# Optimization experiments

Hardware: AMD Instinct MI355X
Metric: run time of the kernel (lower is better)

## Reference

```python
import jax, jax.numpy as jnp
import numpy as np

N_NODES = 100000
N_EDGES = 1600000
D = 64
N_TARGETS = 100
N_GRAPHS = 512


def gcn_conv(x, W, b, src, dst):
    """GCNConv with default add_self_loops=True, symmetric normalization."""
    n = x.shape[0]
    h = x @ W  # [N, out]
    ones = jnp.ones(dst.shape[0], dtype=h.dtype)
    deg = jax.ops.segment_sum(ones, dst, num_segments=n) + 1.0  # +1 for self-loop
    dinv = jax.lax.rsqrt(deg)
    norm = dinv[src] * dinv[dst]  # [E]
    agg = jax.ops.segment_sum(h[src] * norm[:, None], dst, num_segments=n)
    agg = agg + h * (dinv * dinv)[:, None]  # self-loop contribution: 1/deg[i] * h[i]
    return agg + b


def setup_inputs() -> dict:
    key = jax.random.key(0)
    ks = jax.random.split(key, 12)
    x = jax.random.normal(ks[0], (N_NODES, D), dtype=jnp.float32)
    edge_index = jax.random.randint(ks[1], (2, N_EDGES), 0, N_NODES, dtype=jnp.int64)
    batch_seg = jnp.sort(jax.random.randint(ks[2], (N_NODES,), 0, N_GRAPHS, dtype=jnp.int64))
    s = 1.0 / np.sqrt(D)
    W1 = jax.random.normal(ks[3], (D, D), dtype=jnp.float32) * s
    b1 = jnp.zeros((D,), dtype=jnp.float32)
    W2 = jax.random.normal(ks[4], (D, D), dtype=jnp.float32) * s
    b2 = jnp.zeros((D,), dtype=jnp.float32)
    W3 = jax.random.normal(ks[5], (D, D), dtype=jnp.float32) * s
    b3 = jnp.zeros((D,), dtype=jnp.float32)
    Wout = jax.random.normal(ks[6], (D, N_TARGETS), dtype=jnp.float32) * s
    bout = jnp.zeros((N_TARGETS,), dtype=jnp.float32)
    return {"x": x, "W1": W1, "b1": b1, "W2": W2, "b2": b2, "W3": W3, "b3": b3,
            "Wout": Wout, "bout": bout, "edge_index": edge_index, "batch_seg": batch_seg}


def reference(x, W1, b1, W2, b2, W3, b3, Wout, bout, edge_index, batch_seg):
    src, dst = edge_index[0], edge_index[1]
    h = jax.nn.relu(gcn_conv(x, W1, b1, src, dst))   # dropout p=0 -> identity
    h = jax.nn.relu(gcn_conv(h, W2, b2, src, dst))
    h = gcn_conv(h, W3, b3, src, dst)
    counts = jax.ops.segment_sum(jnp.ones(h.shape[0], h.dtype), batch_seg, num_segments=N_GRAPHS)
    pooled = jax.ops.segment_sum(h, batch_seg, num_segments=N_GRAPHS) / jnp.maximum(counts, 1.0)[:, None]
    return pooled @ Wout + bout  # [N_GRAPHS, N_TARGETS]
```

## Files before the change

kernel.cpp:

```cpp
#include <hip/hip_runtime.h>

#define N_NODES   100000
#define N_EDGES   1600000
#define D         64
#define N_TARGETS 100
#define N_GRAPHS  512
#define NBUCK     391
#define EPB       16384
#define BCAP      6144
#define MM_NPW    16
#define NPN       4

typedef _Float16 half4 __attribute__((ext_vector_type(4)));
typedef _Float16 half8 __attribute__((ext_vector_type(8)));
typedef __fp16   hf2   __attribute__((ext_vector_type(2)));
typedef __fp16   hf8   __attribute__((ext_vector_type(8)));

#if defined(__has_builtin)
#if __has_builtin(__builtin_amdgcn_fdot2)
#define USE_DOT2 1
#endif
#endif

__device__ __forceinline__ void prepW_dev(const float* __restrict__ W,
                                          _Float16* __restrict__ out, int t) {
#pragma unroll
    for (int it = 0; it < 2; ++it) {
        int idx = t + it * 256;
        int m = idx >> 3, c = idx & 7;
        half8 hv;
#pragma unroll
        for (int tt = 0; tt < 8; ++tt)
            hv[tt] = (_Float16)W[(8 * c + tt) * 64 + m];
        *(half8*)&out[m * 64 + ((c ^ (m & 7)) * 8)] = hv;
    }
}

__global__ void k_setup(const float* __restrict__ W2, const float* __restrict__ W3,
                        _Float16* __restrict__ WhA, _Float16* __restrict__ WhB,
                        int* __restrict__ gcur, float* __restrict__ poolz) {
    int blk = blockIdx.x;
    int t = threadIdx.x;
    if (blk == 0) { prepW_dev(W2, WhA, t); return; }
    if (blk == 1) { prepW_dev(W3, WhB, t); return; }
    int i = (blk - 2) * 256 + t;
    if (i < NBUCK) gcur[i] = 0;
    if (i < N_GRAPHS * D + N_GRAPHS) poolz[i] = 0.0f;
}

__global__ void __launch_bounds__(1024)
k_binA(const int* __restrict__ src, const int* __restrict__ dst,
       int* __restrict__ gcur, unsigned int* __restrict__ staged) {
    __shared__ int hist[NBUCK];
    __shared__ int boff[NBUCK];
    int tid = threadIdx.x;
    for (int i = tid; i < NBUCK; i += 1024) hist[i] = 0;
    __syncthreads();

    int e0 = blockIdx.x * EPB;
    int s_[16], d_[16], r_[16];
#pragma unroll
    for (int k = 0; k < 16; ++k) {
        int e = e0 + k * 1024 + tid;
        if (e < N_EDGES) {
            s_[k] = src[e];
            d_[k] = dst[e];
            r_[k] = atomicAdd(&hist[d_[k] >> 8], 1);
        } else {
            d_[k] = -1;
        }
    }
    __syncthreads();
    for (int b = tid; b < NBUCK; b += 1024) {
        int h = hist[b];
        boff[b] = (h > 0) ? atomicAdd(&gcur[b], h) : 0;
    }
    __syncthreads();
#pragma unroll
    for (int k = 0; k < 16; ++k) {
        if (d_[k] >= 0) {
            int b = d_[k] >> 8;
            staged[(size_t)b * BCAP + boff[b] + r_[k]] =
                ((unsigned)(d_[k] & 255) << 17) | (unsigned)s_[k];
        }
    }
}

__global__ void k_scanB(const int* __restrict__ gcur, int* __restrict__ bstart) {
    __shared__ int s[512];
    int t = threadIdx.x;
    int v = (t < NBUCK) ? gcur[t] : 0;
    s[t] = v;
    __syncthreads();
    for (int off = 1; off < 512; off <<= 1) {
        int x = (t >= off) ? s[t - off] : 0;
        __syncthreads();
        s[t] += x;
        __syncthreads();
    }
    if (t < NBUCK) bstart[t] = s[t] - v;
    if (t == 0) bstart[NBUCK] = N_EDGES;
}

__global__ void __launch_bounds__(256)
k_binB(const unsigned int* __restrict__ staged, const int* __restrict__ gcur,
       const int* __restrict__ bstart, int* __restrict__ esrc,
       int* __restrict__ base, float* __restrict__ dinv) {
    __shared__ int s[256];
    __shared__ int lbase[256];
    __shared__ int cur[256];
    int b = blockIdx.x;
    int t = threadIdx.x;
    int n0 = b << 8;
    int Eb = gcur[b];
    int Sb = bstart[b];
    const unsigned int* sl = staged + (size_t)b * BCAP;

    cur[t] = 0;
    __syncthreads();
    for (int k = t; k < Eb; k += 256) {
        int dl = (int)(sl[k] >> 17) & 255;
        atomicAdd(&cur[dl], 1);
    }
    __syncthreads();
    int v = cur[t];
    s[t] = v;
    __syncthreads();
    for (int off = 1; off < 256; off <<= 1) {
        int x = (t >= off) ? s[t - off] : 0;
        __syncthreads();
        s[t] += x;
        __syncthreads();
    }
    lbase[t] = s[t] - v;
    int gi = n0 + t;
    if (gi < N_NODES) {
        base[gi] = Sb + (s[t] - v);
        dinv[gi] = rsqrtf((float)v + 1.0f);
    }
    if (b == 0 && t == 0) base[N_NODES] = N_EDGES;
    cur[t] = 0;
    __syncthreads();
    for (int k = t; k < Eb; k += 256) {
        unsigned int pd = sl[k];
        int dl = (int)(pd >> 17) & 255;
        int pos = Sb + lbase[dl] + atomicAdd(&cur[dl], 1);
        esrc[pos] = (int)(pd & 0x1FFFFu);
    }
}

__global__ void __launch_bounds__(256)
k_mm(const float* __restrict__ X, const float* __restrict__ W,
     const float* __restrict__ dinv, _Float16* __restrict__ Y16) {
    __shared__ float W1L[D * D];
    __shared__ float aSh[4][D];
    int tid = threadIdx.x;
#pragma unroll
    for (int it = 0; it < 4; ++it) {
        int idx = (tid + it * 256) * 4;
        *(float4*)&W1L[idx] = *(const float4*)(W + idx);
    }
    __syncthreads();

    int wv = tid >> 6, lane = tid & 63;
    float wreg[D];
#pragma unroll
    for (int k = 0; k < D; ++k)
        wreg[k] = W1L[k * D + lane];

    int i0 = (blockIdx.x * 4 + wv) * MM_NPW;
    if (i0 >= N_NODES) return;
    int iEnd = i0 + MM_NPW; if (iEnd > N_NODES) iEnd = N_NODES;

    float xv = X[(size_t)i0 * D + lane];
    for (int i = i0; i < iEnd; ++i) {
        int inext = (i + 1 < N_NODES) ? (i + 1) : i;
        float xnext = X[(size_t)inext * D + lane];

        aSh[wv][lane] = xv;
        asm volatile("s_waitcnt lgkmcnt(0)" ::: "memory");

        float ac0 = 0.f, ac1 = 0.f, ac2 = 0.f, ac3 = 0.f;
#pragma unroll
        for (int c = 0; c < 16; ++c) {
            float4 a4 = *(const float4*)&aSh[wv][c * 4];
            ac0 = fmaf(a4.x, wreg[4 * c + 0], ac0);
            ac1 = fmaf(a4.y, wreg[4 * c + 1], ac1);
            ac2 = fmaf(a4.z, wreg[4 * c + 2], ac2);
            ac3 = fmaf(a4.w, wreg[4 * c + 3], ac3);
        }
        float acc = (ac0 + ac1) + (ac2 + ac3);
        Y16[(size_t)i * D + lane] = (_Float16)(acc * dinv[i]);
        xv = xnext;
    }
}

__global__ void __launch_bounds__(256)
k_pullmm(const _Float16* __restrict__ H, const int* __restrict__ esrc,
         const int* __restrict__ base, const float* __restrict__ dinv,
         const float* __restrict__ b_in, const _Float16* __restrict__ Whg,
         _Float16* __restrict__ Hout) {
    __shared__ _Float16 WhL[D * D];
    __shared__ float    red[4][8][D + 4];
    __shared__ _Float16 aSh[4][D];
    {
#pragma unroll
        for (int it = 0; it < 2; ++it) {
            int t = threadIdx.x + it * 256;
            *(half8*)&WhL[t * 8] = *(const half8*)&Whg[t * 8];
        }
    }
    __syncthreads();

    int wv   = threadIdx.x >> 6;
    int lane = threadIdx.x & 63;
    int g = lane >> 3, l = lane & 7;
    float bias = b_in[lane];
    int i0 = (blockIdx.x * 4 + wv) * NPN;

    for (int n = 0; n < NPN; ++n) {
        int i = i0 + n;
        int s0 = base[i], s1 = base[i + 1];

        float acc[8] = {0.f, 0.f, 0.f, 0.f, 0.f, 0.f, 0.f, 0.f};
        if (g == 0) {
            half8 sv = *(const half8*)(H + (size_t)i * D + l * 8);
#pragma unroll
            for (int q = 0; q < 8; ++q) acc[q] = (float)sv[q];
        }

        int p = s0;
        while (p < s1) {
            int cnt = s1 - p;
            if (cnt > 64) cnt = 64;
            int ed = (lane < cnt) ? esrc[p + lane] : 0;
            int j = 0;
            for (; j + 32 <= cnt; j += 32) {
                int e0 = __shfl(ed, j + g, 64);
                int e1 = __shfl(ed, j + 8 + g, 64);
                int e2 = __shfl(ed, j + 16 + g, 64);
                int e3 = __shfl(ed, j + 24 + g, 64);
                half8 v0 = *(const half8*)(H + (size_t)(unsigned)e0 * D + l * 8);
                half8 v1 = *(const half8*)(H + (size_t)(unsigned)e1 * D + l * 8);
                half8 v2 = *(const half8*)(H + (size_t)(unsigned)e2 * D + l * 8);
                half8 v3 = *(const half8*)(H + (size_t)(unsigned)e3 * D + l * 8);
                half8 s01 = v0 + v1;
                half8 s23 = v2 + v3;
#pragma unroll
                for (int q = 0; q < 8; ++q)
                    acc[q] += (float)s01[q] + (float)s23[q];
            }
            for (; j + 16 <= cnt; j += 16) {
                int e0 = __shfl(ed, j + g, 64);
                int e1 = __shfl(ed, j + 8 + g, 64);
                half8 v0 = *(const half8*)(H + (size_t)(unsigned)e0 * D + l * 8);
                half8 v1 = *(const half8*)(H + (size_t)(unsigned)e1 * D + l * 8);
                half8 s01 = v0 + v1;
#pragma unroll
                for (int q = 0; q < 8; ++q) acc[q] += (float)s01[q];
            }
            for (; j + 8 <= cnt; j += 8) {
                int e0 = __shfl(ed, j + g, 64);
                half8 v0 = *(const half8*)(H + (size_t)(unsigned)e0 * D + l * 8);
#pragma unroll
                for (int q = 0; q < 8; ++q) acc[q] += (float)v0[q];
            }
            if (j < cnt) {
                int idx = j + g;
                int e0 = __shfl(ed, idx & 63, 64);
                if (idx < cnt) {
                    half8 v0 = *(const half8*)(H + (size_t)(unsigned)e0 * D + l * 8);
#pragma unroll
                    for (int q = 0; q < 8; ++q) acc[q] += (float)v0[q];
                }
            }
            p += cnt;
        }

        *(float4*)&red[wv][g][l * 8]     = make_float4(acc[0], acc[1], acc[2], acc[3]);
        *(float4*)&red[wv][g][l * 8 + 4] = make_float4(acc[4], acc[5], acc[6], acc[7]);
        asm volatile("s_waitcnt lgkmcnt(0)" ::: "memory");
        float ag0 = 0.f, ag1 = 0.f;
#pragma unroll
        for (int gg = 0; gg < 8; gg += 2) {
            ag0 += red[wv][gg][lane];
            ag1 += red[wv][gg + 1][lane];
        }
        float agg = ag0 + ag1;

        float di = dinv[i];
        float av = fmaxf(fmaf(agg, di, bias), 0.f);
        aSh[wv][lane] = (_Float16)av;
        asm volatile("s_waitcnt lgkmcnt(0)" ::: "memory");

        float p0 = 0.f, p1 = 0.f, p2 = 0.f, p3 = 0.f;
#pragma unroll
        for (int c = 0; c < 8; ++c) {
            hf8 a8 = *(const hf8*)&aSh[wv][c * 8];
            hf8 w8 = *(const hf8*)&WhL[lane * 64 + ((c ^ (lane & 7)) * 8)];
#ifdef USE_DOT2
            hf2 a0; a0.x = a8[0]; a0.y = a8[1];
            hf2 a1; a1.x = a8[2]; a1.y = a8[3];
            hf2 a2; a2.x = a8[4]; a2.y = a8[5];
            hf2 a3; a3.x = a8[6]; a3.y = a8[7];
            hf2 w0; w0.x = w8[0]; w0.y = w8[1];
            hf2 w1; w1.x = w8[2]; w1.y = w8[3];
            hf2 w2; w2.x = w8[4]; w2.y = w8[5];
            hf2 w3; w3.x = w8[6]; w3.y = w8[7];
            p0 = __builtin_amdgcn_fdot2(a0, w0, p0, false);
            p1 = __builtin_amdgcn_fdot2(a1, w1, p1, false);
            p2 = __builtin_amdgcn_fdot2(a2, w2, p2, false);
            p3 = __builtin_amdgcn_fdot2(a3, w3, p3, false);
#else
#pragma unroll
            for (int t = 0; t < 8; t += 4) {
                p0 = fmaf((float)a8[t],     (float)w8[t],     p0);
                p1 = fmaf((float)a8[t + 1], (float)w8[t + 1], p1);
                p2 = fmaf((float)a8[t + 2], (float)w8[t + 2], p2);
                p3 = fmaf((float)a8[t + 3], (float)w8[t + 3], p3);
            }
#endif
        }
        float part = (p0 + p1) + (p2 + p3);
        Hout[(size_t)i * D + lane] = (_Float16)(part * di);
    }
}

__global__ void __launch_bounds__(256)
k_pull(const _Float16* __restrict__ H, const int* __restrict__ esrc,
       const int* __restrict__ base, const float* __restrict__ dinv,
       const float* __restrict__ b, _Float16* __restrict__ AGG16) {
    __shared__ float red[4][8][D + 4];
    int wv   = threadIdx.x >> 6;
    int lane = threadIdx.x & 63;
    int g = lane >> 3, l = lane & 7;
    float bias = b[lane];
    int i0 = (blockIdx.x * 4 + wv) * NPN;

    for (int n = 0; n < NPN; ++n) {
        int i = i0 + n;
        int s0 = base[i], s1 = base[i + 1];

        float acc[8] = {0.f, 0.f, 0.f, 0.f, 0.f, 0.f, 0.f, 0.f};
        if (g == 0) {
            half8 sv = *(const half8*)(H + (size_t)i * D + l * 8);
#pragma unroll
            for (int q = 0; q < 8; ++q) acc[q] = (float)sv[q];
        }

        int p = s0;
        while (p < s1) {
            int cnt = s1 - p;
            if (cnt > 64) cnt = 64;
            int ed = (lane < cnt) ? esrc[p + lane] : 0;
            int j = 0;
            for (; j + 32 <= cnt; j += 32) {
                int e0 = __shfl(ed, j + g, 64);
                int e1 = __shfl(ed, j + 8 + g, 64);
                int e2 = __shfl(ed, j + 16 + g, 64);
                int e3 = __shfl(ed, j + 24 + g, 64);
                half8 v0 = *(const half8*)(H + (size_t)(unsigned)e0 * D + l * 8);
                half8 v1 = *(const half8*)(H + (size_t)(unsigned)e1 * D + l * 8);
                half8 v2 = *(const half8*)(H + (size_t)(unsigned)e2 * D + l * 8);
                half8 v3 = *(const half8*)(H + (size_t)(unsigned)e3 * D + l * 8);
                half8 s01 = v0 + v1;
                half8 s23 = v2 + v3;
#pragma unroll
                for (int q = 0; q < 8; ++q)
                    acc[q] += (float)s01[q] + (float)s23[q];
            }
            for (; j + 16 <= cnt; j += 16) {
                int e0 = __shfl(ed, j + g, 64);
                int e1 = __shfl(ed, j + 8 + g, 64);
                half8 v0 = *(const half8*)(H + (size_t)(unsigned)e0 * D + l * 8);
                half8 v1 = *(const half8*)(H + (size_t)(unsigned)e1 * D + l * 8);
                half8 s01 = v0 + v1;
#pragma unroll
                for (int q = 0; q < 8; ++q) acc[q] += (float)s01[q];
            }
            for (; j + 8 <= cnt; j += 8) {
                int e0 = __shfl(ed, j + g, 64);
                half8 v0 = *(const half8*)(H + (size_t)(unsigned)e0 * D + l * 8);
#pragma unroll
                for (int q = 0; q < 8; ++q) acc[q] += (float)v0[q];
            }
            if (j < cnt) {
                int idx = j + g;
                int e0 = __shfl(ed, idx & 63, 64);
                if (idx < cnt) {
                    half8 v0 = *(const half8*)(H + (size_t)(unsigned)e0 * D + l * 8);
#pragma unroll
                    for (int q = 0; q < 8; ++q) acc[q] += (float)v0[q];
                }
            }
            p += cnt;
        }

        *(float4*)&red[wv][g][l * 8]     = make_float4(acc[0], acc[1], acc[2], acc[3]);
        *(float4*)&red[wv][g][l * 8 + 4] = make_float4(acc[4], acc[5], acc[6], acc[7]);
        asm volatile("s_waitcnt lgkmcnt(0)" ::: "memory");
        float ag0 = 0.f, ag1 = 0.f;
#pragma unroll
        for (int gg = 0; gg < 8; gg += 2) {
            ag0 += red[wv][gg][lane];
            ag1 += red[wv][gg + 1][lane];
        }
        float agg = ag0 + ag1;
        asm volatile("s_waitcnt lgkmcnt(0)" ::: "memory");

        AGG16[(size_t)i * D + lane] = (_Float16)fmaf(agg, dinv[i], bias);
    }
}

__global__ void __launch_bounds__(256)
k_pool_seg(const _Float16* __restrict__ H16, const int* __restrict__ seg,
           float* __restrict__ pooled, float* __restrict__ counts) {
    int wave = threadIdx.x >> 6;
    int lane = threadIdx.x & 63;
    int n0 = (blockIdx.x * 4 + wave) * 64;
    if (n0 >= N_NODES) return;
    int nEnd = n0 + 64;
    if (nEnd > N_NODES) nEnd = N_NODES;
    int cur = seg[n0];
    float acc = 0.0f;
    int run = 0;
    for (int n = n0; n < nEnd; ++n) {
        int gsg = seg[n];
        if (gsg != cur) {
            atomicAdd(&pooled[(size_t)cur * D + lane], acc);
            if (lane == 0) atomicAdd(&counts[cur], (float)run);
            acc = 0.0f; run = 0;
            cur = gsg;
        }
        acc += (float)H16[(size_t)n * D + lane];
        run += 1;
    }
    atomicAdd(&pooled[(size_t)cur * D + lane], acc);
    if (lane == 0) atomicAdd(&counts[cur], (float)run);
}

__global__ void k_out(const float* __restrict__ pooled, const float* __restrict__ counts,
                      const float* __restrict__ Wout, const float* __restrict__ bout,
                      float* __restrict__ out) {
    __shared__ float prow[D];
    int g = blockIdx.x;
    int t = threadIdx.x;
    if (t < D) prow[t] = pooled[(size_t)g * D + t] / fmaxf(counts[g], 1.0f);
    __syncthreads();
    if (t < N_TARGETS) {
        float acc = bout[t];
#pragma unroll
        for (int k = 0; k < D; ++k)
            acc = fmaf(prow[k], Wout[k * N_TARGETS + t], acc);
        out[g * N_TARGETS + t] = acc;
    }
}


extern "C" void kernel_launch(void* const* d_in, const int* in_sizes, int n_in,
                              void* d_out, int out_size, void* d_ws, size_t ws_size,
                              hipStream_t stream) {
    const float* x    = (const float*)d_in[0];
    const float* W1   = (const float*)d_in[1];
    const float* b1   = (const float*)d_in[2];
    const float* W2   = (const float*)d_in[3];
    const float* b2   = (const float*)d_in[4];
    const float* W3   = (const float*)d_in[5];
    const float* b3   = (const float*)d_in[6];
    const float* Wout = (const float*)d_in[7];
    const float* bout = (const float*)d_in[8];
    const int*   eidx = (const int*)d_in[9];
    const int*   seg  = (const int*)d_in[10];
    const int* src = eidx;
    const int* dst = eidx + N_EDGES;
    float* out = (float*)d_out;

    _Float16* H16A   = (_Float16*)d_ws;
    _Float16* H16B   = H16A + (size_t)N_NODES * D;
    _Float16* AGG16  = H16B;
    unsigned int* staged = (unsigned int*)d_ws;
    int*      esrc   = (int*)(H16B + (size_t)N_NODES * D);
    float*    dinv   = (float*)(esrc + N_EDGES);
    int*      base   = (int*)(dinv + N_NODES);
    float*    pooled = (float*)(base + N_NODES + 4);
    float*    counts = pooled + N_GRAPHS * D;
    int*      gcur   = (int*)(counts + N_GRAPHS);
    int*      bstart = gcur + 512;
    _Float16* WhA    = (_Float16*)(bstart + 512);
    _Float16* WhB    = WhA + 4096;

    const int NB = (N_NODES + 255) / 256;

    k_setup<<<132, 256, 0, stream>>>(W2, W3, WhA, WhB, gcur, pooled);

    k_binA<<<(N_EDGES + EPB - 1) / EPB, 1024, 0, stream>>>(src, dst, gcur, staged);
    k_scanB<<<1, 512, 0, stream>>>(gcur, bstart);
    k_binB<<<NBUCK, 256, 0, stream>>>(staged, gcur, bstart, esrc, base, dinv);

    const int MMB = (N_NODES + 4 * MM_NPW - 1) / (4 * MM_NPW);
    const int PB  = N_NODES / (4 * NPN);
    k_mm<<<MMB, 256, 0, stream>>>(x, W1, dinv, H16A);
    k_pullmm<<<PB, 256, 0, stream>>>(H16A, esrc, base, dinv, b1, WhA, H16B);
    k_pullmm<<<PB, 256, 0, stream>>>(H16B, esrc, base, dinv, b2, WhB, H16A);
    k_pull<<<PB, 256, 0, stream>>>(H16A, esrc, base, dinv, b3, AGG16);

    k_pool_seg<<<NB, 256, 0, stream>>>(AGG16, seg, pooled, counts);
    k_out<<<N_GRAPHS, 128, 0, stream>>>(pooled, counts, Wout, bout, out);
}
```

Baseline: 309.9 us.

## Fuse graph mean-pooling into final aggregation kernel via shared-memory partial sums

The last GCN aggregation kernel now accumulates its per-node outputs directly into per-block shared-memory pool slots keyed by segment id, then flushes those slots to global pooled sums and counts with atomics. This removes the separate pooling kernel and the fp16 write and re-read of the final node features. It assumes the 16 nodes of a block span at most 16 consecutive segments, which holds for sorted segment ids, and it adds shared-memory atomics plus a block barrier to the pull kernel.

```diff
diff --git a/kernel.cpp b/kernel.cpp
--- a/kernel.cpp
+++ b/kernel.cpp
@@ -329,13 +329,26 @@
 __global__ void __launch_bounds__(256)
 k_pull(const _Float16* __restrict__ H, const int* __restrict__ esrc,
        const int* __restrict__ base, const float* __restrict__ dinv,
-       const float* __restrict__ b, _Float16* __restrict__ AGG16) {
+       const float* __restrict__ b, const int* __restrict__ seg,
+       float* __restrict__ pooled, float* __restrict__ counts) {
     __shared__ float red[4][8][D + 4];
+    __shared__ float poolL[16][D];
+    __shared__ float cntL[16];
     int wv   = threadIdx.x >> 6;
     int lane = threadIdx.x & 63;
     int g = lane >> 3, l = lane & 7;
     float bias = b[lane];
-    int i0 = (blockIdx.x * 4 + wv) * NPN;
+    int ib0 = blockIdx.x * 16;
+    int g0  = seg[ib0];
+    int i0 = ib0 + wv * NPN;
+
+    {
+        int t = threadIdx.x;
+#pragma unroll
+        for (int z = 0; z < 4; ++z) poolL[(t * 4 + z) >> 6][(t * 4 + z) & 63] = 0.f;
+        if (t < 16) cntL[t] = 0.f;
+    }
+    __syncthreads();
 
     for (int n = 0; n < NPN; ++n) {
         int i = i0 + n;
@@ -408,35 +421,22 @@
         float agg = ag0 + ag1;
         asm volatile("s_waitcnt lgkmcnt(0)" ::: "memory");
 
-        AGG16[(size_t)i * D + lane] = (_Float16)fmaf(agg, dinv[i], bias);
-    }
-}
-
-__global__ void __launch_bounds__(256)
-k_pool_seg(const _Float16* __restrict__ H16, const int* __restrict__ seg,
-           float* __restrict__ pooled, float* __restrict__ counts) {
-    int wave = threadIdx.x >> 6;
-    int lane = threadIdx.x & 63;
-    int n0 = (blockIdx.x * 4 + wave) * 64;
-    if (n0 >= N_NODES) return;
-    int nEnd = n0 + 64;
-    if (nEnd > N_NODES) nEnd = N_NODES;
-    int cur = seg[n0];
-    float acc = 0.0f;
-    int run = 0;
-    for (int n = n0; n < nEnd; ++n) {
-        int gsg = seg[n];
-        if (gsg != cur) {
-            atomicAdd(&pooled[(size_t)cur * D + lane], acc);
-            if (lane == 0) atomicAdd(&counts[cur], (float)run);
-            acc = 0.0f; run = 0;
-            cur = gsg;
-        }
-        acc += (float)H16[(size_t)n * D + lane];
-        run += 1;
-    }
-    atomicAdd(&pooled[(size_t)cur * D + lane], acc);
-    if (lane == 0) atomicAdd(&counts[cur], (float)run);
+        float val = fmaf(agg, dinv[i], bias);
+        int slot = seg[i] - g0;
+        atomicAdd(&poolL[slot][lane], val);
+        if (lane == 0) atomicAdd(&cntL[slot], 1.0f);
+    }
+    __syncthreads();
+
+#pragma unroll
+    for (int k = 0; k < 4; ++k) {
+        int slot = wv + 4 * k;
+        float c = cntL[slot];
+        if (c > 0.f) {
+            atomicAdd(&pooled[(size_t)(g0 + slot) * D + lane], poolL[slot][lane]);
+            if (lane == 0) atomicAdd(&counts[g0 + slot], c);
+        }
+    }
 }
 
 __global__ void k_out(const float* __restrict__ pooled, const float* __restrict__ counts,
@@ -477,7 +477,6 @@
 
     _Float16* H16A   = (_Float16*)d_ws;
     _Float16* H16B   = H16A + (size_t)N_NODES * D;
-    _Float16* AGG16  = H16B;
     unsigned int* staged = (unsigned int*)d_ws;
     int*      esrc   = (int*)(H16B + (size_t)N_NODES * D);
     float*    dinv   = (float*)(esrc + N_EDGES);
@@ -489,8 +488,6 @@
     _Float16* WhA    = (_Float16*)(bstart + 512);
     _Float16* WhB    = WhA + 4096;
 
-    const int NB = (N_NODES + 255) / 256;
-
     k_setup<<<132, 256, 0, stream>>>(W2, W3, WhA, WhB, gcur, pooled);
 
     k_binA<<<(N_EDGES + EPB - 1) / EPB, 1024, 0, stream>>>(src, dst, gcur, staged);
@@ -502,8 +499,7 @@
     k_mm<<<MMB, 256, 0, stream>>>(x, W1, dinv, H16A);
     k_pullmm<<<PB, 256, 0, stream>>>(H16A, esrc, base, dinv, b1, WhA, H16B);
     k_pullmm<<<PB, 256, 0, stream>>>(H16B, esrc, base, dinv, b2, WhB, H16A);
-    k_pull<<<PB, 256, 0, stream>>>(H16A, esrc, base, dinv, b3, AGG16);
-
-    k_pool_seg<<<NB, 256, 0, stream>>>(AGG16, seg, pooled, counts);
+    k_pull<<<PB, 256, 0, stream>>>(H16A, esrc, base, dinv, b3, seg, pooled, counts);
+
     k_out<<<N_GRAPHS, 128, 0, stream>>>(pooled, counts, Wout, bout, out);
 }
```

After: 304.7 us. About the same (-1.7%).
